# Performance work log

Hardware: AMD Instinct MI355X
Metric: run time of the kernel (lower is better)

Reference implementation:

```python
import jax, jax.numpy as jnp
import numpy as np
from jax import lax

DIM = 192
HEADS = 4
HIDDEN = int(DIM * 2.66)  # 510
B, H, W = 2, 64, 64
EPS_LN = 1e-6
EPS_NORM = 1e-12


def conv1x1(x, w, b):
    # x: (b,c,h,w), w: (o,c), b: (o,)
    return jnp.einsum('bchw,oc->bohw', x, w) + b[None, :, None, None]


def dwconv3x3(x, w, b):
    # depthwise 3x3, SAME padding; w: (C,1,3,3)
    c = x.shape[1]
    y = lax.conv_general_dilated(x, w, window_strides=(1, 1), padding='SAME',
                                 feature_group_count=c,
                                 dimension_numbers=('NCHW', 'OIHW', 'NCHW'))
    return y + b[None, :, None, None]


def layernorm2d(x, w, b):
    mean = jnp.mean(x, axis=(2, 3), keepdims=True)
    var = jnp.mean((x - mean) ** 2, axis=(2, 3), keepdims=True)
    return (x - mean) / jnp.sqrt(var + EPS_LN) * w[None, :, None, None] + b[None, :, None, None]


def mdta(x, qkv_w, qkv_b, qkv_dw_w, qkv_dw_b, temperature, proj_w, proj_b):
    b, c, h, w = x.shape
    qkv = dwconv3x3(conv1x1(x, qkv_w, qkv_b), qkv_dw_w, qkv_dw_b)
    q, k, v = jnp.split(qkv, 3, axis=1)
    dh = c // HEADS
    q = q.reshape(b, HEADS, dh, h * w)
    k = k.reshape(b, HEADS, dh, h * w)
    v = v.reshape(b, HEADS, dh, h * w)
    # L2-normalize over per-head channel dim (axis=2), like F.normalize(dim=2)
    q = q / jnp.maximum(jnp.linalg.norm(q, axis=2, keepdims=True), EPS_NORM)
    k = k / jnp.maximum(jnp.linalg.norm(k, axis=2, keepdims=True), EPS_NORM)
    # spatial attention map: (b, heads, HW, HW)
    attn = jnp.einsum('bhcn,bhcm->bhnm', q, k) * temperature[None]  # temp (heads,1,1)
    attn = jax.nn.softmax(attn, axis=-1)
    out = jnp.einsum('bhnm,bhcm->bhcn', attn, v)  # (b,heads,dh,HW)
    out = out.reshape(b, c, h, w)
    return conv1x1(out, proj_w, proj_b)


def gdfn(x, pin_w, pin_b, dw_w, dw_b, pout_w, pout_b):
    y = dwconv3x3(conv1x1(x, pin_w, pin_b), dw_w, dw_b)
    y1, y2 = jnp.split(y, 2, axis=1)
    y = jax.nn.gelu(y1, approximate=False) * y2
    return conv1x1(y, pout_w, pout_b)


def setup_inputs() -> dict:
    key = jax.random.key(0)
    ks = jax.random.split(key, 8)
    s = 0.02
    return {
        'x': jax.random.normal(ks[0], (B, DIM, H, W), jnp.float32),
        'ln1_w': jnp.ones((DIM,), jnp.float32),
        'ln1_b': jnp.zeros((DIM,), jnp.float32),
        'qkv_w': jax.random.normal(ks[1], (DIM * 3, DIM), jnp.float32) * s,
        'qkv_b': jnp.zeros((DIM * 3,), jnp.float32),
        'qkv_dw_w': jax.random.normal(ks[2], (DIM * 3, 1, 3, 3), jnp.float32) * s,
        'qkv_dw_b': jnp.zeros((DIM * 3,), jnp.float32),
        'temperature': jnp.ones((HEADS, 1, 1), jnp.float32),
        'proj_w': jax.random.normal(ks[3], (DIM, DIM), jnp.float32) * s,
        'proj_b': jnp.zeros((DIM,), jnp.float32),
        'ln2_w': jnp.ones((DIM,), jnp.float32),
        'ln2_b': jnp.zeros((DIM,), jnp.float32),
        'pin_w': jax.random.normal(ks[4], (HIDDEN * 2, DIM), jnp.float32) * s,
        'pin_b': jnp.zeros((HIDDEN * 2,), jnp.float32),
        'gdfn_dw_w': jax.random.normal(ks[5], (HIDDEN * 2, 1, 3, 3), jnp.float32) * s,
        'gdfn_dw_b': jnp.zeros((HIDDEN * 2,), jnp.float32),
        'pout_w': jax.random.normal(ks[6], (DIM, HIDDEN), jnp.float32) * s,
        'pout_b': jnp.zeros((DIM,), jnp.float32),
    }


def reference(x, ln1_w, ln1_b, qkv_w, qkv_b, qkv_dw_w, qkv_dw_b, temperature,
              proj_w, proj_b, ln2_w, ln2_b, pin_w, pin_b, gdfn_dw_w, gdfn_dw_b,
              pout_w, pout_b):
    x = x + mdta(layernorm2d(x, ln1_w, ln1_b), qkv_w, qkv_b, qkv_dw_w, qkv_dw_b,
                 temperature, proj_w, proj_b)
    x = x + gdfn(layernorm2d(x, ln2_w, ln2_b), pin_w, pin_b, gdfn_dw_w, gdfn_dw_b,
                 pout_w, pout_b)
    return x
```

## Files before the change

### kernel.cpp

```cpp
#include <hip/hip_runtime.h>
#include <hip/hip_bf16.h>

typedef __bf16 bf16x8 __attribute__((ext_vector_type(8)));
typedef __bf16 bf16x4 __attribute__((ext_vector_type(4)));
typedef __bf16 bf16x2 __attribute__((ext_vector_type(2)));
typedef float f32x4 __attribute__((ext_vector_type(4)));

#define HW 4096
#define DIMC 192
#define DH 48
#define HIDC 510
#define LOG2E 1.44269504088896f

__global__ void wcvt4_kernel(const float* __restrict__ qkv_w, const float* __restrict__ proj_w,
                             const float* __restrict__ pin_w, const float* __restrict__ pout_w,
                             __bf16* __restrict__ wb_qkv, __bf16* __restrict__ wb_proj,
                             __bf16* __restrict__ wb_pin, __bf16* __restrict__ wb_pout) {
  int idx = blockIdx.x * 256 + threadIdx.x;
  if (idx < 110592) {
    wb_qkv[idx] = (__bf16)qkv_w[idx];
  } else if (idx < 147456) {
    int i = idx - 110592;
    wb_proj[i] = (__bf16)proj_w[i];
  } else if (idx < 343296) {
    int i = idx - 147456;
    wb_pin[i] = (__bf16)pin_w[i];
  } else if (idx < 441600) {
    int i = idx - 343296;
    int o = i >> 9, c = i & 511;
    wb_pout[i] = (c < HIDC) ? (__bf16)pout_w[o * HIDC + c] : (__bf16)0.f;
  }
}

__global__ __launch_bounds__(256) void ln_stats_kernel(const float* __restrict__ x, const float* __restrict__ w,
                                                       const float* __restrict__ b, float* __restrict__ sc,
                                                       float* __restrict__ sh) {
  int bc = blockIdx.x;
  int c = bc % DIMC;
  const float* row = x + (size_t)bc * HW;
  float s = 0.f, s2 = 0.f;
  for (int i = threadIdx.x * 4; i < HW; i += 1024) {
    f32x4 v = *(const f32x4*)&row[i];
    s += (v.x + v.y) + (v.z + v.w);
    s2 = fmaf(v.x, v.x, s2); s2 = fmaf(v.y, v.y, s2);
    s2 = fmaf(v.z, v.z, s2); s2 = fmaf(v.w, v.w, s2);
  }
  __shared__ float red[8];
  for (int off = 32; off; off >>= 1) { s += __shfl_down(s, off, 64); s2 += __shfl_down(s2, off, 64); }
  int wid = threadIdx.x >> 6;
  if ((threadIdx.x & 63) == 0) { red[wid] = s; red[4 + wid] = s2; }
  __syncthreads();
  if (threadIdx.x == 0) {
    s = red[0] + red[1] + red[2] + red[3];
    s2 = red[4] + red[5] + red[6] + red[7];
    float mean = s * (1.f / HW);
    float var = s2 * (1.f / HW) - mean * mean;
    float rstd = rsqrtf(var + 1e-6f);
    float scv = rstd * w[c];
    sc[bc] = scv;
    sh[bc] = b[c] - mean * scv;
  }
}

__global__ __launch_bounds__(256) void ln_apply_t_kernel(const float* __restrict__ x, const float* __restrict__ sc,
                                                         const float* __restrict__ sh, __bf16* __restrict__ Xt) {
  int n0 = blockIdx.x * 64, c0 = blockIdx.y * 32, b = blockIdx.z;
  int t = threadIdx.x;
  int n = t & 63, cs = c0 + (t >> 6) * 8;
  __bf16 ob[8];
#pragma unroll
  for (int cc = 0; cc < 8; ++cc) {
    int c = cs + cc;
    float v = fmaf(x[((size_t)(b * DIMC + c)) * HW + n0 + n], sc[b * DIMC + c], sh[b * DIMC + c]);
    ob[cc] = (__bf16)v;
  }
  *(bf16x8*)&Xt[((size_t)((b << 12) + n0 + n)) * DIMC + cs] = *(bf16x8*)ob;
}

__global__ __launch_bounds__(256) void gemm_kernel(const __bf16* __restrict__ A, const __bf16* __restrict__ Bt,
                                                   const float* __restrict__ bias, const float* __restrict__ res,
                                                   float* __restrict__ outf, __bf16* __restrict__ outb,
                                                   int O, int Cs, int mode) {
  __shared__ __align__(16) __bf16 Asub[64 * 72];
  __shared__ __align__(16) __bf16 Bsub[128 * 72];
  const int t = threadIdx.x;
  const int lane = t & 63, wv = t >> 6;
  const int q4 = lane >> 4, l16 = lane & 15;
  int o0 = blockIdx.y * 64;
  if (o0 + 64 > O) o0 = O - 64;
  const int ntot0 = blockIdx.x * 128;
  const int b = ntot0 >> 12;
  const int n_in_b0 = ntot0 & 4095;

  f32x4 acc[8];
#pragma unroll
  for (int nt = 0; nt < 8; ++nt) acc[nt] = (f32x4){0.f, 0.f, 0.f, 0.f};

  for (int c0 = 0; c0 < Cs; c0 += 64) {
    __syncthreads();
#pragma unroll
    for (int j = 0; j < 2; ++j) {
      int id = t + 256 * j;
      *(bf16x8*)&Asub[(id >> 3) * 72 + (id & 7) * 8] =
          *(const bf16x8*)&A[((size_t)(o0 + (id >> 3))) * Cs + c0 + (id & 7) * 8];
    }
    if (mode != 3) {
#pragma unroll
      for (int j = 0; j < 4; ++j) {
        int id = t + 256 * j;
        *(bf16x8*)&Bsub[(id >> 3) * 72 + (id & 7) * 8] =
            *(const bf16x8*)&Bt[((size_t)(ntot0 + (id >> 3))) * Cs + c0 + (id & 7) * 8];
      }
    } else {
      int cr = t >> 2, seg = t & 3;
      int cg = c0 + cr;
      __bf16 tmp[32];
      if (cg < HIDC) {
        const __bf16* gp = Bt + ((size_t)(b * HIDC + cg)) * HW + n_in_b0 + seg * 32;
#pragma unroll
        for (int j = 0; j < 4; ++j) *(bf16x8*)&tmp[8 * j] = *(const bf16x8*)&gp[8 * j];
      } else {
#pragma unroll
        for (int k = 0; k < 32; ++k) tmp[k] = (__bf16)0.f;
      }
#pragma unroll
      for (int k = 0; k < 32; ++k) Bsub[(seg * 32 + k) * 72 + cr] = tmp[k];
    }
    __syncthreads();
#pragma unroll
    for (int ks = 0; ks < 2; ++ks) {
      bf16x8 af = *(const bf16x8*)&Asub[(16 * wv + l16) * 72 + 32 * ks + 8 * q4];
#pragma unroll
      for (int nt = 0; nt < 8; ++nt) {
        bf16x8 bfr = *(const bf16x8*)&Bsub[(16 * nt + l16) * 72 + 32 * ks + 8 * q4];
        acc[nt] = __builtin_amdgcn_mfma_f32_16x16x32_bf16(af, bfr, acc[nt], 0, 0, 0);
      }
    }
  }

  float bvals[4];
#pragma unroll
  for (int r = 0; r < 4; ++r) bvals[r] = bias[o0 + 16 * wv + 4 * q4 + r];
#pragma unroll
  for (int nt = 0; nt < 8; ++nt) {
    int n_in_b = n_in_b0 + 16 * nt + l16;
#pragma unroll
    for (int r = 0; r < 4; ++r) {
      int o = o0 + 16 * wv + 4 * q4 + r;
      size_t addr = ((size_t)(b * O + o)) * HW + n_in_b;
      float v = acc[nt][r] + bvals[r];
      if (mode >= 2) { outf[addr] = v + res[addr]; }
      else if (mode == 0) { outf[addr] = v; }
      else { outb[addr] = (__bf16)v; }
    }
  }
}

__global__ __launch_bounds__(256) void dwconv_split_kernel(const __bf16* __restrict__ in, const float* __restrict__ w,
                                                           const float* __restrict__ bias,
                                                           __bf16* __restrict__ qdwb, __bf16* __restrict__ Vbf) {
  int bc = blockIdx.x;
  int b = bc / 576, ch = bc - b * 576;
  __shared__ float tile[66 * 68];
  for (int i = threadIdx.x; i < 66 * 68; i += 256) tile[i] = 0.f;
  __syncthreads();
  const __bf16* p = in + (size_t)bc * HW;
  for (int j = 0; j < 8; ++j) {
    int i = 2 * threadIdx.x + 512 * j;
    bf16x2 v = *(const bf16x2*)&p[i];
    int y = i >> 6, xx = i & 63;
    tile[(y + 1) * 68 + xx + 1] = (float)v.x;
    tile[(y + 1) * 68 + xx + 2] = (float)v.y;
  }
  __syncthreads();
  float w0 = w[ch * 9 + 0], w1 = w[ch * 9 + 1], w2 = w[ch * 9 + 2];
  float w3 = w[ch * 9 + 3], w4 = w[ch * 9 + 4], w5 = w[ch * 9 + 5];
  float w6 = w[ch * 9 + 6], w7 = w[ch * 9 + 7], w8 = w[ch * 9 + 8];
  float bb = bias[ch];
  __bf16* dst;
  if (ch < 384) dst = qdwb + ((size_t)(b * 384 + ch)) * HW;
  else {
    int c = ch - 384, h = c / DH, cc = c - h * DH;
    dst = Vbf + ((size_t)((b * 4 + h) * DH + cc)) * HW;
  }
  for (int j = 0; j < 8; ++j) {
    int i = 2 * threadIdx.x + 512 * j;
    int y = i >> 6, xx = i & 63;
    const float* tt = &tile[y * 68 + xx];
    float a = bb;
    a = fmaf(w0, tt[0], a);   a = fmaf(w1, tt[1], a);   a = fmaf(w2, tt[2], a);
    a = fmaf(w3, tt[68], a);  a = fmaf(w4, tt[69], a);  a = fmaf(w5, tt[70], a);
    a = fmaf(w6, tt[136], a); a = fmaf(w7, tt[137], a); a = fmaf(w8, tt[138], a);
    float a2 = bb;
    a2 = fmaf(w0, tt[1], a2);   a2 = fmaf(w1, tt[2], a2);   a2 = fmaf(w2, tt[3], a2);
    a2 = fmaf(w3, tt[69], a2);  a2 = fmaf(w4, tt[70], a2);  a2 = fmaf(w5, tt[71], a2);
    a2 = fmaf(w6, tt[137], a2); a2 = fmaf(w7, tt[138], a2); a2 = fmaf(w8, tt[139], a2);
    bf16x2 o = { (__bf16)a, (__bf16)a2 };
    *(bf16x2*)&dst[i] = o;
  }
}

__global__ __launch_bounds__(256) void gdfn_dw_gate_kernel(const __bf16* __restrict__ hid, const float* __restrict__ w,
                                                           const float* __restrict__ bias, __bf16* __restrict__ gate) {
  int blk = blockIdx.x;
  int b = blk / HIDC, j = blk - b * HIDC;
  __shared__ float t1[66 * 68];
  __shared__ float t2[66 * 68];
  for (int i = threadIdx.x; i < 66 * 68; i += 256) { t1[i] = 0.f; t2[i] = 0.f; }
  __syncthreads();
  const __bf16* p1 = hid + ((size_t)b * (2 * HIDC) + j) * HW;
  const __bf16* p2 = p1 + (size_t)HIDC * HW;
  for (int jj = 0; jj < 8; ++jj) {
    int i = 2 * threadIdx.x + 512 * jj;
    bf16x2 v1 = *(const bf16x2*)&p1[i];
    bf16x2 v2 = *(const bf16x2*)&p2[i];
    int y = i >> 6, xx = i & 63;
    t1[(y + 1) * 68 + xx + 1] = (float)v1.x;
    t1[(y + 1) * 68 + xx + 2] = (float)v1.y;
    t2[(y + 1) * 68 + xx + 1] = (float)v2.x;
    t2[(y + 1) * 68 + xx + 2] = (float)v2.y;
  }
  __syncthreads();
  int c1 = j, c2 = j + HIDC;
  float a0 = w[c1*9+0], a1w = w[c1*9+1], a2w = w[c1*9+2], a3 = w[c1*9+3], a4 = w[c1*9+4],
        a5 = w[c1*9+5], a6 = w[c1*9+6], a7 = w[c1*9+7], a8 = w[c1*9+8];
  float b0 = w[c2*9+0], b1 = w[c2*9+1], b2 = w[c2*9+2], b3 = w[c2*9+3], b4 = w[c2*9+4],
        b5 = w[c2*9+5], b6 = w[c2*9+6], b7 = w[c2*9+7], b8 = w[c2*9+8];
  float bi1 = bias[c1], bi2 = bias[c2];
  __bf16* op = gate + ((size_t)b * HIDC + j) * HW;
  for (int jj = 0; jj < 8; ++jj) {
    int i = 2 * threadIdx.x + 512 * jj;
    int y = i >> 6, xx = i & 63;
    const float* u = &t1[y * 68 + xx];
    const float* v = &t2[y * 68 + xx];
    float x1 = bi1;
    x1 = fmaf(a0, u[0], x1);   x1 = fmaf(a1w, u[1], x1);  x1 = fmaf(a2w, u[2], x1);
    x1 = fmaf(a3, u[68], x1);  x1 = fmaf(a4, u[69], x1);  x1 = fmaf(a5, u[70], x1);
    x1 = fmaf(a6, u[136], x1); x1 = fmaf(a7, u[137], x1); x1 = fmaf(a8, u[138], x1);
    float x1b = bi1;
    x1b = fmaf(a0, u[1], x1b);   x1b = fmaf(a1w, u[2], x1b);  x1b = fmaf(a2w, u[3], x1b);
    x1b = fmaf(a3, u[69], x1b);  x1b = fmaf(a4, u[70], x1b);  x1b = fmaf(a5, u[71], x1b);
    x1b = fmaf(a6, u[137], x1b); x1b = fmaf(a7, u[138], x1b); x1b = fmaf(a8, u[139], x1b);
    float x2 = bi2;
    x2 = fmaf(b0, v[0], x2);   x2 = fmaf(b1, v[1], x2);   x2 = fmaf(b2, v[2], x2);
    x2 = fmaf(b3, v[68], x2);  x2 = fmaf(b4, v[69], x2);  x2 = fmaf(b5, v[70], x2);
    x2 = fmaf(b6, v[136], x2); x2 = fmaf(b7, v[137], x2); x2 = fmaf(b8, v[138], x2);
    float x2b = bi2;
    x2b = fmaf(b0, v[1], x2b);   x2b = fmaf(b1, v[2], x2b);   x2b = fmaf(b2, v[3], x2b);
    x2b = fmaf(b3, v[69], x2b);  x2b = fmaf(b4, v[70], x2b);  x2b = fmaf(b5, v[71], x2b);
    x2b = fmaf(b6, v[137], x2b); x2b = fmaf(b7, v[138], x2b); x2b = fmaf(b8, v[139], x2b);
    float g  = 0.5f * x1  * (1.f + erff(x1  * 0.70710678118654752f));
    float gb = 0.5f * x1b * (1.f + erff(x1b * 0.70710678118654752f));
    bf16x2 o = { (__bf16)(g * x2), (__bf16)(gb * x2b) };
    *(bf16x2*)&op[i] = o;
  }
}

__global__ __launch_bounds__(256) void prep_qk_kernel(const __bf16* __restrict__ qdwb, const float* __restrict__ temp,
                                                      __bf16* __restrict__ Qbf, __bf16* __restrict__ Kbf) {
  int t2 = blockIdx.x * 256 + threadIdx.x;
  int bh = t2 >> 11;
  int np = (t2 & 2047) * 2;
  int b = bh >> 2, h = bh & 3;
  const __bf16* qp = qdwb + ((size_t)(b * 384 + h * DH)) * HW + np;
  const __bf16* kp = qp + (size_t)192 * HW;
  float tq = temp[h] * LOG2E;

  bf16x2 raw[DH];
  float ss0 = 0.f, ss1 = 0.f;
#pragma unroll
  for (int c = 0; c < DH; ++c) {
    bf16x2 v = *(const bf16x2*)&qp[(size_t)c * HW];
    raw[c] = v;
    float f0 = (float)v.x, f1 = (float)v.y;
    ss0 = fmaf(f0, f0, ss0);
    ss1 = fmaf(f1, f1, ss1);
  }
  float sc0 = tq / fmaxf(sqrtf(ss0), 1e-12f);
  float sc1 = tq / fmaxf(sqrtf(ss1), 1e-12f);
  __bf16 ob0[64], ob1[64];
#pragma unroll
  for (int c = 0; c < DH; ++c) {
    ob0[c] = (__bf16)((float)raw[c].x * sc0);
    ob1[c] = (__bf16)((float)raw[c].y * sc1);
  }
#pragma unroll
  for (int c = DH; c < 64; ++c) { ob0[c] = (__bf16)0.f; ob1[c] = (__bf16)0.f; }
  __bf16* qd = Qbf + ((size_t)(bh << 12) + np) * 64;
#pragma unroll
  for (int ch = 0; ch < 8; ++ch) {
    *(bf16x8*)&qd[ch * 8] = *(bf16x8*)&ob0[ch * 8];
    *(bf16x8*)&qd[64 + ch * 8] = *(bf16x8*)&ob1[ch * 8];
  }

  ss0 = 0.f; ss1 = 0.f;
#pragma unroll
  for (int c = 0; c < DH; ++c) {
    bf16x2 v = *(const bf16x2*)&kp[(size_t)c * HW];
    raw[c] = v;
    float f0 = (float)v.x, f1 = (float)v.y;
    ss0 = fmaf(f0, f0, ss0);
    ss1 = fmaf(f1, f1, ss1);
  }
  sc0 = 1.f / fmaxf(sqrtf(ss0), 1e-12f);
  sc1 = 1.f / fmaxf(sqrtf(ss1), 1e-12f);
#pragma unroll
  for (int c = 0; c < DH; ++c) {
    ob0[c] = (__bf16)((float)raw[c].x * sc0);
    ob1[c] = (__bf16)((float)raw[c].y * sc1);
  }
  __bf16* kd = Kbf + ((size_t)(bh << 12) + np) * 64;
#pragma unroll
  for (int ch = 0; ch < 8; ++ch) {
    *(bf16x8*)&kd[ch * 8] = *(bf16x8*)&ob0[ch * 8];
    *(bf16x8*)&kd[64 + ch * 8] = *(bf16x8*)&ob1[ch * 8];
  }
}

__global__ __launch_bounds__(256) void attn_split_kernel(const __bf16* __restrict__ Qbf, const __bf16* __restrict__ Kbf,
                                                         const __bf16* __restrict__ Vbf, float* __restrict__ part) {
  __shared__ __align__(16) __bf16 Kt[64 * 72];
  __shared__ __align__(16) __bf16 Vc[48 * 72];
  __shared__ __align__(16) __bf16 Pl[64 * 72];
  const int tid = threadIdx.x;
  const int lane = tid & 63;
  const int wv = tid >> 6;
  const int q4 = lane >> 4, l16 = lane & 15;
  const int bid = blockIdx.x;
  const int chunk = bid >> 9, rest = bid & 511;
  const int bh = rest >> 6, nt = rest & 63;
  const int n0 = nt * 64;
  const __bf16* Qg = Qbf + (size_t)bh * HW * 64;
  const __bf16* Kg = Kbf + (size_t)bh * HW * 64;
  const __bf16* Vg = Vbf + (size_t)bh * DH * HW;

  bf16x8 qf[4][2];
#pragma unroll
  for (int s = 0; s < 4; ++s)
#pragma unroll
    for (int ks = 0; ks < 2; ++ks)
      qf[s][ks] = *(const bf16x8*)&Qg[((size_t)(n0 + 16 * s + l16)) * 64 + 32 * ks + 8 * q4];

  bf16x8 kreg[2], vreg[2];
  {
    const int m0 = chunk * 16 * 64;
#pragma unroll
    for (int j = 0; j < 2; ++j) {
      int id = tid + 256 * j;
      kreg[j] = *(const bf16x8*)&Kg[((size_t)(m0 + (id >> 3))) * 64 + (id & 7) * 8];
    }
    vreg[0] = *(const bf16x8*)&Vg[((size_t)(tid >> 3)) * HW + m0 + (tid & 7) * 8];
    if (tid < 128) {
      int i = tid + 256;
      vreg[1] = *(const bf16x8*)&Vg[((size_t)(i >> 3)) * HW + m0 + (i & 7) * 8];
    }
  }

  float lsub[4] = {0.f, 0.f, 0.f, 0.f};
  f32x4 oacc[3];
#pragma unroll
  for (int ct = 0; ct < 3; ++ct) oacc[ct] = (f32x4){0.f, 0.f, 0.f, 0.f};

  const int mt_end = chunk * 16 + 16;
  for (int mt = chunk * 16; mt < mt_end; ++mt) {
    __syncthreads();
#pragma unroll
    for (int j = 0; j < 2; ++j) {
      int id = tid + 256 * j;
      *(bf16x8*)&Kt[(id >> 3) * 72 + (id & 7) * 8] = kreg[j];
    }
    *(bf16x8*)&Vc[(tid >> 3) * 72 + (tid & 7) * 8] = vreg[0];
    if (tid < 128) {
      int i = tid + 256;
      *(bf16x8*)&Vc[(i >> 3) * 72 + (i & 7) * 8] = vreg[1];
    }
    if (mt + 1 < mt_end) {
      const int m1 = (mt + 1) * 64;
#pragma unroll
      for (int j = 0; j < 2; ++j) {
        int id = tid + 256 * j;
        kreg[j] = *(const bf16x8*)&Kg[((size_t)(m1 + (id >> 3))) * 64 + (id & 7) * 8];
      }
      vreg[0] = *(const bf16x8*)&Vg[((size_t)(tid >> 3)) * HW + m1 + (tid & 7) * 8];
      if (tid < 128) {
        int i = tid + 256;
        vreg[1] = *(const bf16x8*)&Vg[((size_t)(i >> 3)) * HW + m1 + (i & 7) * 8];
      }
    }
    __syncthreads();

    f32x4 sacc[4];
#pragma unroll
    for (int s = 0; s < 4; ++s) sacc[s] = (f32x4){0.f, 0.f, 0.f, 0.f};
#pragma unroll
    for (int ks = 0; ks < 2; ++ks) {
      bf16x8 af = *(const bf16x8*)&Kt[(16 * wv + l16) * 72 + 32 * ks + 8 * q4];
#pragma unroll
      for (int s = 0; s < 4; ++s)
        sacc[s] = __builtin_amdgcn_mfma_f32_16x16x32_bf16(af, qf[s][ks], sacc[s], 0, 0, 0);
    }

#pragma unroll
    for (int s = 0; s < 4; ++s) {
      float p0 = exp2f(sacc[s][0]);
      float p1 = exp2f(sacc[s][1]);
      float p2 = exp2f(sacc[s][2]);
      float p3 = exp2f(sacc[s][3]);
      lsub[s] += (p0 + p1) + (p2 + p3);
      bf16x4 pk = { (__bf16)p0, (__bf16)p1, (__bf16)p2, (__bf16)p3 };
      *(bf16x4*)&Pl[(16 * s + l16) * 72 + 16 * wv + 4 * q4] = pk;
    }
    __syncthreads();

#pragma unroll
    for (int ks = 0; ks < 2; ++ks) {
      bf16x8 pf = *(const bf16x8*)&Pl[(16 * wv + l16) * 72 + 32 * ks + 8 * q4];
#pragma unroll
      for (int ct = 0; ct < 3; ++ct) {
        bf16x8 vf = *(const bf16x8*)&Vc[(16 * ct + l16) * 72 + 32 * ks + 8 * q4];
        oacc[ct] = __builtin_amdgcn_mfma_f32_16x16x32_bf16(pf, vf, oacc[ct], 0, 0, 0);
      }
    }
  }

  __syncthreads();
  float* Lred = (float*)Kt;
#pragma unroll
  for (int s = 0; s < 4; ++s) {
    float v = lsub[s];
    v += __shfl_xor(v, 16, 64);
    v += __shfl_xor(v, 32, 64);
    if (q4 == 0) Lred[wv * 64 + 16 * s + l16] = v;
  }
  __syncthreads();
  size_t pbase = (size_t)bid * 3136;
  if (tid < 64)
    part[pbase + 3072 + tid] = Lred[tid] + Lred[64 + tid] + Lred[128 + tid] + Lred[192 + tid];
#pragma unroll
  for (int ct = 0; ct < 3; ++ct)
#pragma unroll
    for (int r = 0; r < 4; ++r) {
      int n = 16 * wv + 4 * q4 + r;
      part[pbase + (size_t)n * 48 + 16 * ct + l16] = oacc[ct][r];
    }
}

__global__ __launch_bounds__(256) void attn_merge_kernel(const float* __restrict__ part, __bf16* __restrict__ Xt) {
  const int bid = blockIdx.x;
  const int bh = bid >> 6, nt = bid & 63;
  const int b = bh >> 2, h = bh & 3;
  const int n0 = nt * 64;
  const int t = threadIdx.x;
  __shared__ float linv[64];
  if (t < 64) {
    float s = 0.f;
#pragma unroll
    for (int ch = 0; ch < 4; ++ch) s += part[((size_t)(ch * 512 + bid)) * 3136 + 3072 + t];
    linv[t] = 1.f / s;
  }
  __syncthreads();
#pragma unroll
  for (int j = 0; j < 3; ++j) {
    int id = t + 256 * j;
    int n = id / 12, cc = (id - n * 12) * 4;
    f32x4 s = (f32x4){0.f, 0.f, 0.f, 0.f};
#pragma unroll
    for (int ch = 0; ch < 4; ++ch) s += *(const f32x4*)&part[((size_t)(ch * 512 + bid)) * 3136 + (size_t)n * 48 + cc];
    float li = linv[n];
    bf16x4 ov = { (__bf16)(s.x * li), (__bf16)(s.y * li), (__bf16)(s.z * li), (__bf16)(s.w * li) };
    *(bf16x4*)&Xt[((size_t)((b << 12) + n0 + n)) * DIMC + h * DH + cc] = ov;
  }
}

extern "C" void kernel_launch(void* const* d_in, const int* in_sizes, int n_in,
                              void* d_out, int out_size, void* d_ws, size_t ws_size,
                              hipStream_t stream) {
  const float* x        = (const float*)d_in[0];
  const float* ln1_w    = (const float*)d_in[1];
  const float* ln1_b    = (const float*)d_in[2];
  const float* qkv_w    = (const float*)d_in[3];
  const float* qkv_b    = (const float*)d_in[4];
  const float* qkv_dw_w = (const float*)d_in[5];
  const float* qkv_dw_b = (const float*)d_in[6];
  const float* temperature = (const float*)d_in[7];
  const float* proj_w   = (const float*)d_in[8];
  const float* proj_b   = (const float*)d_in[9];
  const float* ln2_w    = (const float*)d_in[10];
  const float* ln2_b    = (const float*)d_in[11];
  const float* pin_w    = (const float*)d_in[12];
  const float* pin_b    = (const float*)d_in[13];
  const float* gdfn_dw_w = (const float*)d_in[14];
  const float* gdfn_dw_b = (const float*)d_in[15];
  const float* pout_w   = (const float*)d_in[16];
  const float* pout_b   = (const float*)d_in[17];
  float* out = (float*)d_out;
  float* ws = (float*)d_ws;

  __bf16* wb_qkv  = (__bf16*)(ws + 0);
  __bf16* wb_proj = (__bf16*)(ws + 55296);
  __bf16* wb_pin  = (__bf16*)(ws + 73728);
  __bf16* wb_pout = (__bf16*)(ws + 171648);
  float* sc1 = ws + 220800;
  float* sh1 = ws + 221184;
  float* sc2 = ws + 221568;
  float* sh2 = ws + 221952;
  __bf16* Xt1 = (__bf16*)(ws + 222336);
  __bf16* Xt2 = (__bf16*)(ws + 222336);
  __bf16* Qbf = (__bf16*)(ws + 222336);
  __bf16* Kbf = (__bf16*)(ws + 1270912);
  __bf16* Vbf = (__bf16*)(ws + 2319488);
  __bf16* qkvb   = (__bf16*)(ws + 3105920);
  __bf16* Xt_att = (__bf16*)(ws + 3105920);
  __bf16* hid    = (__bf16*)(ws + 3105920);
  __bf16* qdwb  = (__bf16*)(ws + 5465216);
  float*  Opart = ws + 5465216;
  __bf16* gate  = (__bf16*)(ws + 7283840);

  wcvt4_kernel<<<1725, 256, 0, stream>>>(qkv_w, proj_w, pin_w, pout_w, wb_qkv, wb_proj, wb_pin, wb_pout);

  ln_stats_kernel<<<2 * DIMC, 256, 0, stream>>>(x, ln1_w, ln1_b, sc1, sh1);
  ln_apply_t_kernel<<<dim3(64, 6, 2), 256, 0, stream>>>(x, sc1, sh1, Xt1);
  gemm_kernel<<<dim3(64, 9), 256, 0, stream>>>(wb_qkv, Xt1, qkv_b, nullptr, nullptr, qkvb, 576, 192, 1);
  dwconv_split_kernel<<<1152, 256, 0, stream>>>(qkvb, qkv_dw_w, qkv_dw_b, qdwb, Vbf);
  prep_qk_kernel<<<64, 256, 0, stream>>>(qdwb, temperature, Qbf, Kbf);
  attn_split_kernel<<<2048, 256, 0, stream>>>(Qbf, Kbf, Vbf, Opart);
  attn_merge_kernel<<<512, 256, 0, stream>>>(Opart, Xt_att);
  gemm_kernel<<<dim3(64, 3), 256, 0, stream>>>(wb_proj, Xt_att, proj_b, x, out, nullptr, 192, 192, 2);

  ln_stats_kernel<<<2 * DIMC, 256, 0, stream>>>(out, ln2_w, ln2_b, sc2, sh2);
  ln_apply_t_kernel<<<dim3(64, 6, 2), 256, 0, stream>>>(out, sc2, sh2, Xt2);
  gemm_kernel<<<dim3(64, 16), 256, 0, stream>>>(wb_pin, Xt2, pin_b, nullptr, nullptr, hid, 1020, 192, 1);
  gdfn_dw_gate_kernel<<<2 * HIDC, 256, 0, stream>>>(hid, gdfn_dw_w, gdfn_dw_b, gate);
  gemm_kernel<<<dim3(64, 3), 256, 0, stream>>>(wb_pout, (const __bf16*)gate, pout_b, out, out, nullptr, 192, 512, 3);
}
```

Baseline: 260.1 us.

## Split Q/K prep across grid, break MFMA dependency chains, fix gate-load coalescing

prep_qk now launches a second grid dimension so Q and K normalization run in separate blocks, doubling parallelism of a tiny 64-block launch. In the attention kernel, the score and PV MFMAs use two independent accumulators per k-step (summed afterwards) and are wrapped in s_setprio, so back-to-back dependent MFMAs can overlap. The mode-3 GEMM B-tile load remaps threads so consecutive threads read consecutive channels rather than segments. Costs are extra accumulator registers and an additional add per output.

```diff
diff --git a/kernel.cpp b/kernel.cpp
--- a/kernel.cpp
+++ b/kernel.cpp
@@ -112,7 +112,7 @@
             *(const bf16x8*)&Bt[((size_t)(ntot0 + (id >> 3))) * Cs + c0 + (id & 7) * 8];
       }
     } else {
-      int cr = t >> 2, seg = t & 3;
+      int cr = t & 63, seg = t >> 6;
       int cg = c0 + cr;
       __bf16 tmp[32];
       if (cg < HIDC) {
@@ -262,15 +262,15 @@
   int bh = t2 >> 11;
   int np = (t2 & 2047) * 2;
   int b = bh >> 2, h = bh & 3;
-  const __bf16* qp = qdwb + ((size_t)(b * 384 + h * DH)) * HW + np;
-  const __bf16* kp = qp + (size_t)192 * HW;
-  float tq = temp[h] * LOG2E;
+  const int isK = blockIdx.y;
+  const __bf16* sp = qdwb + ((size_t)(b * 384 + isK * 192 + h * DH)) * HW + np;
+  float tq = isK ? 1.f : temp[h] * LOG2E;
 
   bf16x2 raw[DH];
   float ss0 = 0.f, ss1 = 0.f;
 #pragma unroll
   for (int c = 0; c < DH; ++c) {
-    bf16x2 v = *(const bf16x2*)&qp[(size_t)c * HW];
+    bf16x2 v = *(const bf16x2*)&sp[(size_t)c * HW];
     raw[c] = v;
     float f0 = (float)v.x, f1 = (float)v.y;
     ss0 = fmaf(f0, f0, ss0);
@@ -286,34 +286,11 @@
   }
 #pragma unroll
   for (int c = DH; c < 64; ++c) { ob0[c] = (__bf16)0.f; ob1[c] = (__bf16)0.f; }
-  __bf16* qd = Qbf + ((size_t)(bh << 12) + np) * 64;
+  __bf16* dd = (isK ? Kbf : Qbf) + ((size_t)(bh << 12) + np) * 64;
 #pragma unroll
   for (int ch = 0; ch < 8; ++ch) {
-    *(bf16x8*)&qd[ch * 8] = *(bf16x8*)&ob0[ch * 8];
-    *(bf16x8*)&qd[64 + ch * 8] = *(bf16x8*)&ob1[ch * 8];
-  }
-
-  ss0 = 0.f; ss1 = 0.f;
-#pragma unroll
-  for (int c = 0; c < DH; ++c) {
-    bf16x2 v = *(const bf16x2*)&kp[(size_t)c * HW];
-    raw[c] = v;
-    float f0 = (float)v.x, f1 = (float)v.y;
-    ss0 = fmaf(f0, f0, ss0);
-    ss1 = fmaf(f1, f1, ss1);
-  }
-  sc0 = 1.f / fmaxf(sqrtf(ss0), 1e-12f);
-  sc1 = 1.f / fmaxf(sqrtf(ss1), 1e-12f);
-#pragma unroll
-  for (int c = 0; c < DH; ++c) {
-    ob0[c] = (__bf16)((float)raw[c].x * sc0);
-    ob1[c] = (__bf16)((float)raw[c].y * sc1);
-  }
-  __bf16* kd = Kbf + ((size_t)(bh << 12) + np) * 64;
-#pragma unroll
-  for (int ch = 0; ch < 8; ++ch) {
-    *(bf16x8*)&kd[ch * 8] = *(bf16x8*)&ob0[ch * 8];
-    *(bf16x8*)&kd[64 + ch * 8] = *(bf16x8*)&ob1[ch * 8];
+    *(bf16x8*)&dd[ch * 8] = *(bf16x8*)&ob0[ch * 8];
+    *(bf16x8*)&dd[64 + ch * 8] = *(bf16x8*)&ob1[ch * 8];
   }
 }
 
@@ -357,9 +334,11 @@
   }
 
   float lsub[4] = {0.f, 0.f, 0.f, 0.f};
-  f32x4 oacc[3];
-#pragma unroll
-  for (int ct = 0; ct < 3; ++ct) oacc[ct] = (f32x4){0.f, 0.f, 0.f, 0.f};
+  f32x4 oacc[2][3];
+#pragma unroll
+  for (int ks = 0; ks < 2; ++ks)
+#pragma unroll
+    for (int ct = 0; ct < 3; ++ct) oacc[ks][ct] = (f32x4){0.f, 0.f, 0.f, 0.f};
 
   const int mt_end = chunk * 16 + 16;
   for (int mt = chunk * 16; mt < mt_end; ++mt) {
@@ -389,38 +368,48 @@
     }
     __syncthreads();
 
-    f32x4 sacc[4];
-#pragma unroll
-    for (int s = 0; s < 4; ++s) sacc[s] = (f32x4){0.f, 0.f, 0.f, 0.f};
-#pragma unroll
-    for (int ks = 0; ks < 2; ++ks) {
-      bf16x8 af = *(const bf16x8*)&Kt[(16 * wv + l16) * 72 + 32 * ks + 8 * q4];
-#pragma unroll
-      for (int s = 0; s < 4; ++s)
-        sacc[s] = __builtin_amdgcn_mfma_f32_16x16x32_bf16(af, qf[s][ks], sacc[s], 0, 0, 0);
-    }
+    bf16x8 af0 = *(const bf16x8*)&Kt[(16 * wv + l16) * 72 + 8 * q4];
+    bf16x8 af1 = *(const bf16x8*)&Kt[(16 * wv + l16) * 72 + 32 + 8 * q4];
+    f32x4 sacc[2][4];
+#pragma unroll
+    for (int ks = 0; ks < 2; ++ks)
+#pragma unroll
+      for (int s = 0; s < 4; ++s) sacc[ks][s] = (f32x4){0.f, 0.f, 0.f, 0.f};
+    __builtin_amdgcn_s_setprio(1);
+#pragma unroll
+    for (int s = 0; s < 4; ++s)
+      sacc[0][s] = __builtin_amdgcn_mfma_f32_16x16x32_bf16(af0, qf[s][0], sacc[0][s], 0, 0, 0);
+#pragma unroll
+    for (int s = 0; s < 4; ++s)
+      sacc[1][s] = __builtin_amdgcn_mfma_f32_16x16x32_bf16(af1, qf[s][1], sacc[1][s], 0, 0, 0);
+    __builtin_amdgcn_s_setprio(0);
 
 #pragma unroll
     for (int s = 0; s < 4; ++s) {
-      float p0 = exp2f(sacc[s][0]);
-      float p1 = exp2f(sacc[s][1]);
-      float p2 = exp2f(sacc[s][2]);
-      float p3 = exp2f(sacc[s][3]);
+      float p0 = exp2f(sacc[0][s][0] + sacc[1][s][0]);
+      float p1 = exp2f(sacc[0][s][1] + sacc[1][s][1]);
+      float p2 = exp2f(sacc[0][s][2] + sacc[1][s][2]);
+      float p3 = exp2f(sacc[0][s][3] + sacc[1][s][3]);
       lsub[s] += (p0 + p1) + (p2 + p3);
       bf16x4 pk = { (__bf16)p0, (__bf16)p1, (__bf16)p2, (__bf16)p3 };
       *(bf16x4*)&Pl[(16 * s + l16) * 72 + 16 * wv + 4 * q4] = pk;
     }
     __syncthreads();
 
-#pragma unroll
-    for (int ks = 0; ks < 2; ++ks) {
-      bf16x8 pf = *(const bf16x8*)&Pl[(16 * wv + l16) * 72 + 32 * ks + 8 * q4];
-#pragma unroll
-      for (int ct = 0; ct < 3; ++ct) {
-        bf16x8 vf = *(const bf16x8*)&Vc[(16 * ct + l16) * 72 + 32 * ks + 8 * q4];
-        oacc[ct] = __builtin_amdgcn_mfma_f32_16x16x32_bf16(pf, vf, oacc[ct], 0, 0, 0);
-      }
-    }
+    bf16x8 pf0 = *(const bf16x8*)&Pl[(16 * wv + l16) * 72 + 8 * q4];
+    bf16x8 pf1 = *(const bf16x8*)&Pl[(16 * wv + l16) * 72 + 32 + 8 * q4];
+    __builtin_amdgcn_s_setprio(1);
+#pragma unroll
+    for (int ct = 0; ct < 3; ++ct) {
+      bf16x8 vf = *(const bf16x8*)&Vc[(16 * ct + l16) * 72 + 8 * q4];
+      oacc[0][ct] = __builtin_amdgcn_mfma_f32_16x16x32_bf16(pf0, vf, oacc[0][ct], 0, 0, 0);
+    }
+#pragma unroll
+    for (int ct = 0; ct < 3; ++ct) {
+      bf16x8 vf = *(const bf16x8*)&Vc[(16 * ct + l16) * 72 + 32 + 8 * q4];
+      oacc[1][ct] = __builtin_amdgcn_mfma_f32_16x16x32_bf16(pf1, vf, oacc[1][ct], 0, 0, 0);
+    }
+    __builtin_amdgcn_s_setprio(0);
   }
 
   __syncthreads();
@@ -441,7 +430,7 @@
 #pragma unroll
     for (int r = 0; r < 4; ++r) {
       int n = 16 * wv + 4 * q4 + r;
-      part[pbase + (size_t)n * 48 + 16 * ct + l16] = oacc[ct][r];
+      part[pbase + (size_t)n * 48 + 16 * ct + l16] = oacc[0][ct][r] + oacc[1][ct][r];
     }
 }
 
@@ -522,7 +511,7 @@
   ln_apply_t_kernel<<<dim3(64, 6, 2), 256, 0, stream>>>(x, sc1, sh1, Xt1);
   gemm_kernel<<<dim3(64, 9), 256, 0, stream>>>(wb_qkv, Xt1, qkv_b, nullptr, nullptr, qkvb, 576, 192, 1);
   dwconv_split_kernel<<<1152, 256, 0, stream>>>(qkvb, qkv_dw_w, qkv_dw_b, qdwb, Vbf);
-  prep_qk_kernel<<<64, 256, 0, stream>>>(qdwb, temperature, Qbf, Kbf);
+  prep_qk_kernel<<<dim3(64, 2), 256, 0, stream>>>(qdwb, temperature, Qbf, Kbf);
   attn_split_kernel<<<2048, 256, 0, stream>>>(Qbf, Kbf, Vbf, Opart);
   attn_merge_kernel<<<512, 256, 0, stream>>>(Opart, Xt_att);
   gemm_kernel<<<dim3(64, 3), 256, 0, stream>>>(wb_proj, Xt_att, proj_b, x, out, nullptr, 192, 192, 2);
```

After: 262.9 us. About the same (+1.1%).
